# Performance work log

Measured on AMD Instinct MI355X. Metric: run time of the kernel, lower is better.

Reference implementation:

```python
import jax, jax.numpy as jnp
import numpy as np

INTRA_K = 16
OUTER_K = 16
MAX_PAIR = 1024


def _mahalanobis(x, cov_inv, mean):
    # x: (..., D) difference vectors; returns squared Mahalanobis-style form (...,)
    xc = x - mean
    return jnp.einsum('...i,ij,...j->...', xc, cov_inv, xc)


def setup_inputs() -> dict:
    key = jax.random.key(0)
    k1, k2, k3 = jax.random.split(key, 3)
    B, N, M = 4, 1024, 1024
    outputs = jax.random.normal(k1, (B, N, 9), dtype=jnp.float32)
    targets = jax.random.normal(k2, (B, M, 9), dtype=jnp.float32)
    mask = jax.random.randint(k3, (B, M), 0, 2).astype(bool)
    return {"outputs": outputs, "targets": targets, "mask": mask}


def reference(outputs, targets, mask):
    y_pred = outputs[:, :MAX_PAIR]                      # (B, N, 9)
    m = mask.astype(y_pred.dtype)                       # (B, M)
    cnt = m.sum()

    # mean / covariance over masked true grasps (equivalent to boolean-gather)
    mean = (targets * m[..., None]).sum((0, 1)) / cnt   # (9,)
    centered = (targets - mean) * m[..., None]          # masked rows contribute 0
    flat = centered.reshape(-1, 9)
    cov = flat.T @ flat / (cnt - 1.0)                   # (9, 9)
    cov_inv = jnp.linalg.pinv(cov)

    # intra loss: true-vs-pred pairwise distances, masked rows excluded
    diff = targets[:, :, None, :] - y_pred[:, None, :, :]   # (B, M, N, 9)
    d = _mahalanobis(diff, cov_inv, mean)                   # (B, M, N)
    neg_topk, _ = jax.lax.top_k(-d, INTRA_K)                # k smallest
    row_sum = (-neg_topk).sum(-1)                           # (B, M)
    intra_loss = (row_sum * m).sum() / cnt                  # mean over masked rows

    # outer loss: pred-vs-pred pairwise distances, no mask
    diff_r = y_pred[:, None, :, :] - y_pred[:, :, None, :]  # (B, N, N, 9); [b,i,j] = pred[b,j]-pred[b,i]
    d_r = _mahalanobis(diff_r, cov_inv, mean)               # (B, N, N)
    neg_tk, _ = jax.lax.top_k(-d_r, OUTER_K)
    outer_loss = (-neg_tk).mean()

    return intra_loss, intra_loss, outer_loss
```

## Files before the change

### kernel.cpp

```cpp
#include <hip/hip_runtime.h>
#include <math.h>

#define BB   4
#define MM   1024
#define NN   1024
#define DD   9
#define KSEL 16
#define NROW (BB * MM)
#define NSLOT (2 * NROW)
#define NBLK (NSLOT / 4)

struct Ws {
  float yT[BB * DD * NN];
  float qy[BB * NN];
  float rowsum[NSLOT];
  float part[16][55];
  float cnt;
  float mean[DD];
  float cinv[DD * DD];
};

__global__ __launch_bounds__(256) void stats_kernel(
    const float* __restrict__ targets, const int* __restrict__ mask,
    Ws* __restrict__ ws) {
  const int tid = threadIdx.x;
  const int r = blockIdx.x * 256 + tid;

  float acc[55];
#pragma unroll
  for (int k = 0; k < 55; ++k) acc[k] = 0.f;
  if (mask[r] != 0) {
    float t[DD];
#pragma unroll
    for (int k = 0; k < DD; ++k) t[k] = targets[r * DD + k];
    acc[0] = 1.f;
#pragma unroll
    for (int k = 0; k < DD; ++k) acc[1 + k] = t[k];
    int u = 10;
#pragma unroll
    for (int p = 0; p < DD; ++p)
#pragma unroll
      for (int q = p; q < DD; ++q) acc[u++] = t[p] * t[q];
  }

  __shared__ float lds[4][55];
#pragma unroll
  for (int k = 0; k < 55; ++k) {
    float v = acc[k];
#pragma unroll
    for (int off = 32; off > 0; off >>= 1) v += __shfl_down(v, off, 64);
    if ((tid & 63) == 0) lds[tid >> 6][k] = v;
  }
  __syncthreads();
  if (tid < 55)
    ws->part[blockIdx.x][tid] =
        lds[0][tid] + lds[1][tid] + lds[2][tid] + lds[3][tid];
}

__global__ __launch_bounds__(256) void prep_kernel(
    const float* __restrict__ outputs, Ws* __restrict__ ws) {
  const int tid = threadIdx.x;
  __shared__ double Sd[55];
  __shared__ float Cs[DD * DD];

  if (tid < 55) {
    double s = 0.0;
#pragma unroll
    for (int b = 0; b < 16; ++b) s += (double)ws->part[b][tid];
    Sd[tid] = s;
  }
  __syncthreads();

  if (tid < 64) {
    const int lane = tid;
    const double cnt = Sd[0];
    const int p = (lane < DD) ? lane : 0;
    double row[2 * DD];
    {
      const double mu_p = Sd[1 + p] / cnt;
#pragma unroll
      for (int q = 0; q < DD; ++q) {
        const int pp = (p < q) ? p : q;
        const int qq = (p < q) ? q : p;
        const int idx = 10 + 9 * pp - (pp * (pp - 1)) / 2 + (qq - pp);
        row[q] = (Sd[idx] - cnt * mu_p * (Sd[1 + q] / cnt)) / (cnt - 1.0);
        row[DD + q] = (p == q) ? 1.0 : 0.0;
      }
    }
#pragma unroll
    for (int c = 0; c < DD; ++c) {
      const double diag = __shfl(row[c], c, 64);
      const double dinv = 1.0 / diag;
      if (lane == c) {
#pragma unroll
        for (int q = 0; q < 2 * DD; ++q) row[q] *= dinv;
      }
      const double f = (lane == c) ? 0.0 : row[c];
#pragma unroll
      for (int q = 0; q < 2 * DD; ++q) {
        const double pv = __shfl(row[q], c, 64);
        row[q] -= f * pv;
      }
    }
    if (lane < DD) {
#pragma unroll
      for (int q = 0; q < DD; ++q) {
        const float cf = (float)row[DD + q];
        Cs[lane * DD + q] = cf;
        if (blockIdx.x == 0) ws->cinv[lane * DD + q] = cf;
      }
    }
    if (lane == 0 && blockIdx.x == 0) {
      ws->cnt = (float)cnt;
#pragma unroll
      for (int q = 0; q < DD; ++q) ws->mean[q] = (float)(Sd[1 + q] / cnt);
    }
  }
  __syncthreads();

  const int j = blockIdx.x * 256 + tid;
  const int b = j >> 10;
  const int jj = j & (NN - 1);
  float C[DD * DD];
#pragma unroll
  for (int k = 0; k < DD * DD; ++k) C[k] = Cs[k];
  float y[DD];
#pragma unroll
  for (int k = 0; k < DD; ++k) y[k] = outputs[j * DD + k];
  float q = 0.f;
#pragma unroll
  for (int p = 0; p < DD; ++p) {
    float s = 0.f;
#pragma unroll
    for (int t = 0; t < DD; ++t) s += C[p * DD + t] * y[t];
    q += y[p] * s;
    ws->yT[(b * DD + p) * NN + jj] = y[p];
  }
  ws->qy[j] = q;
}

__global__ __launch_bounds__(256) void dist_kernel(
    const float* __restrict__ outputs, const float* __restrict__ targets,
    const int* __restrict__ mask, Ws* __restrict__ ws) {
  const int wv = threadIdx.x >> 6;
  const int lane = threadIdx.x & 63;
  const int s = blockIdx.x * 4 + wv;
  const bool is_intra = (s < NROW);
  const int r = s & (NROW - 1);
  const int b = r >> 10;

  if (is_intra && mask[r] == 0) {
    if (lane == 0) ws->rowsum[s] = 0.f;
    return;
  }

  float a[DD];
  if (is_intra) {
#pragma unroll
    for (int k = 0; k < DD; ++k) a[k] = targets[r * DD + k] - ws->mean[k];
  } else {
#pragma unroll
    for (int k = 0; k < DD; ++k) a[k] = outputs[r * DD + k] + ws->mean[k];
  }
  float w[DD];
  float qa = 0.f;
#pragma unroll
  for (int p = 0; p < DD; ++p) {
    float acc = 0.f;
#pragma unroll
    for (int t = 0; t < DD; ++t) acc += ws->cinv[p * DD + t] * a[t];
    w[p] = acc;
    qa += a[p] * acc;
  }

  float v[16];
#pragma unroll
  for (int k = 0; k < 16; ++k) v[k] = 0.f;
  const float* __restrict__ yTb = ws->yT + (size_t)b * DD * NN;
#pragma unroll
  for (int p = 0; p < DD; ++p) {
    const float4* __restrict__ pl = (const float4*)(yTb + (size_t)p * NN);
#pragma unroll
    for (int c = 0; c < 4; ++c) {
      const float4 y4 = pl[c * 64 + lane];
      v[c * 4 + 0] += w[p] * y4.x;
      v[c * 4 + 1] += w[p] * y4.y;
      v[c * 4 + 2] += w[p] * y4.z;
      v[c * 4 + 3] += w[p] * y4.w;
    }
  }
  {
    const float4* __restrict__ q4 = (const float4*)(ws->qy + (size_t)b * NN);
#pragma unroll
    for (int c = 0; c < 4; ++c) {
      const float4 qv = q4[c * 64 + lane];
      v[c * 4 + 0] = qa + qv.x - 2.f * v[c * 4 + 0];
      v[c * 4 + 1] = qa + qv.y - 2.f * v[c * 4 + 1];
      v[c * 4 + 2] = qa + qv.z - 2.f * v[c * 4 + 2];
      v[c * 4 + 3] = qa + qv.w - 2.f * v[c * 4 + 3];
    }
  }

#pragma unroll
  for (int k = 2; k <= 16; k <<= 1) {
#pragma unroll
    for (int j = k >> 1; j > 0; j >>= 1) {
#pragma unroll
      for (int i = 0; i < 16; ++i) {
        const int l = i ^ j;
        if (l > i) {
          const bool up = ((i & k) == 0);
          const float lo = fminf(v[i], v[l]);
          const float hi = fmaxf(v[i], v[l]);
          v[i] = up ? lo : hi;
          v[l] = up ? hi : lo;
        }
      }
    }
  }

#pragma unroll
  for (int off = 1; off < 64; off <<= 1) {
    float pr[16];
#pragma unroll
    for (int i = 0; i < 16; ++i) pr[i] = __shfl_xor(v[i], off, 64);
#pragma unroll
    for (int i = 0; i < 16; ++i) v[i] = fminf(v[i], pr[15 - i]);
    if (off < 32) {
#pragma unroll
      for (int j = 8; j > 0; j >>= 1) {
#pragma unroll
        for (int i = 0; i < 16; ++i) {
          const int l = i ^ j;
          if (l > i) {
            const float lo = fminf(v[i], v[l]);
            const float hi = fmaxf(v[i], v[l]);
            v[i] = lo;
            v[l] = hi;
          }
        }
      }
    }
  }

  float total = v[0];
#pragma unroll
  for (int k = 1; k < 16; ++k) total += v[k];
  if (lane == 0) ws->rowsum[s] = total;
}

__global__ __launch_bounds__(256) void finalize_kernel(
    const Ws* __restrict__ ws, float* __restrict__ out) {
  const int tid = threadIdx.x;
  double li = 0.0, lo = 0.0;
  for (int k = tid; k < NROW; k += 256) {
    li += (double)ws->rowsum[k];
    lo += (double)ws->rowsum[NROW + k];
  }
#pragma unroll
  for (int off = 32; off > 0; off >>= 1) {
    li += __shfl_down(li, off, 64);
    lo += __shfl_down(lo, off, 64);
  }
  __shared__ double lds_i[4], lds_o[4];
  if ((tid & 63) == 0) {
    lds_i[tid >> 6] = li;
    lds_o[tid >> 6] = lo;
  }
  __syncthreads();
  if (tid == 0) {
    const double si = lds_i[0] + lds_i[1] + lds_i[2] + lds_i[3];
    const double so = lds_o[0] + lds_o[1] + lds_o[2] + lds_o[3];
    const float intra = (float)(si / (double)ws->cnt);
    const float outer = (float)(so / (double)(NROW * KSEL));
    out[0] = intra;
    out[1] = intra;
    out[2] = outer;
  }
}

extern "C" void kernel_launch(void* const* d_in, const int* in_sizes, int n_in,
                              void* d_out, int out_size, void* d_ws,
                              size_t ws_size, hipStream_t stream) {
  const float* outputs = (const float*)d_in[0];
  const float* targets = (const float*)d_in[1];
  const int* mask = (const int*)d_in[2];
  Ws* ws = (Ws*)d_ws;
  float* out = (float*)d_out;

  stats_kernel<<<NROW / 256, 256, 0, stream>>>(targets, mask, ws);
  prep_kernel<<<(BB * NN) / 256, 256, 0, stream>>>(outputs, ws);
  dist_kernel<<<NBLK, 256, 0, stream>>>(outputs, targets, mask, ws);
  finalize_kernel<<<1, 256, 0, stream>>>(ws, out);
}
```

Baseline: 97.23 us.

## Fuse intra/outer rows per wave and fold finalize into dist kernel via ticket

Each wave now handles one target row and one prediction row together, so every load of the transposed predictions and the quadratic terms feeds both distance sets. The separate finalize kernel is replaced by a last-block-done ticket reduction inside the distance kernel, saving a launch. Masked intra rows are no longer skipped early; their top-k is computed and then zeroed, which adds some work. Register pressure roughly doubles, with two 16-value arrays per lane, which may reduce occupancy.

```diff
diff --git a/kernel.cpp b/kernel.cpp
--- a/kernel.cpp
+++ b/kernel.cpp
@@ -1,23 +1,24 @@
 #include <hip/hip_runtime.h>
 #include <math.h>
 
-#define BB   4
-#define MM   1024
-#define NN   1024
-#define DD   9
-#define KSEL 16
-#define NROW (BB * MM)
-#define NSLOT (2 * NROW)
-#define NBLK (NSLOT / 4)
+#define BB    4
+#define MM    1024
+#define NN    1024
+#define DD    9
+#define KSEL  16
+#define NROW  (BB * MM)
+#define NBLKD (NROW / 4)
 
 struct Ws {
   float yT[BB * DD * NN];
   float qy[BB * NN];
-  float rowsum[NSLOT];
+  float bpart_i[NBLKD];
+  float bpart_o[NBLKD];
   float part[16][55];
   float cnt;
   float mean[DD];
   float cinv[DD * DD];
+  unsigned ticket;
 };
 
 __global__ __launch_bounds__(256) void stats_kernel(
@@ -25,6 +26,7 @@
     Ws* __restrict__ ws) {
   const int tid = threadIdx.x;
   const int r = blockIdx.x * 256 + tid;
+  if (blockIdx.x == 0 && tid == 0) ws->ticket = 0u;
 
   float acc[55];
 #pragma unroll
@@ -72,9 +74,8 @@
   __syncthreads();
 
   if (tid < 64) {
-    const int lane = tid;
     const double cnt = Sd[0];
-    const int p = (lane < DD) ? lane : 0;
+    const int p = (tid < DD) ? tid : 0;
     double row[2 * DD];
     {
       const double mu_p = Sd[1 + p] / cnt;
@@ -91,26 +92,26 @@
     for (int c = 0; c < DD; ++c) {
       const double diag = __shfl(row[c], c, 64);
       const double dinv = 1.0 / diag;
-      if (lane == c) {
+      if (tid == c) {
 #pragma unroll
         for (int q = 0; q < 2 * DD; ++q) row[q] *= dinv;
       }
-      const double f = (lane == c) ? 0.0 : row[c];
+      const double f = (tid == c) ? 0.0 : row[c];
 #pragma unroll
       for (int q = 0; q < 2 * DD; ++q) {
         const double pv = __shfl(row[q], c, 64);
         row[q] -= f * pv;
       }
     }
-    if (lane < DD) {
+    if (tid < DD) {
 #pragma unroll
       for (int q = 0; q < DD; ++q) {
         const float cf = (float)row[DD + q];
-        Cs[lane * DD + q] = cf;
-        if (blockIdx.x == 0) ws->cinv[lane * DD + q] = cf;
-      }
-    }
-    if (lane == 0 && blockIdx.x == 0) {
+        Cs[tid * DD + q] = cf;
+        if (blockIdx.x == 0) ws->cinv[tid * DD + q] = cf;
+      }
+    }
+    if (tid == 0 && blockIdx.x == 0) {
       ws->cnt = (float)cnt;
 #pragma unroll
       for (int q = 0; q < DD; ++q) ws->mean[q] = (float)(Sd[1 + q] / cnt);
@@ -121,9 +122,6 @@
   const int j = blockIdx.x * 256 + tid;
   const int b = j >> 10;
   const int jj = j & (NN - 1);
-  float C[DD * DD];
-#pragma unroll
-  for (int k = 0; k < DD * DD; ++k) C[k] = Cs[k];
   float y[DD];
 #pragma unroll
   for (int k = 0; k < DD; ++k) y[k] = outputs[j * DD + k];
@@ -132,75 +130,14 @@
   for (int p = 0; p < DD; ++p) {
     float s = 0.f;
 #pragma unroll
-    for (int t = 0; t < DD; ++t) s += C[p * DD + t] * y[t];
+    for (int t = 0; t < DD; ++t) s += Cs[p * DD + t] * y[t];
     q += y[p] * s;
     ws->yT[(b * DD + p) * NN + jj] = y[p];
   }
   ws->qy[j] = q;
 }
 
-__global__ __launch_bounds__(256) void dist_kernel(
-    const float* __restrict__ outputs, const float* __restrict__ targets,
-    const int* __restrict__ mask, Ws* __restrict__ ws) {
-  const int wv = threadIdx.x >> 6;
-  const int lane = threadIdx.x & 63;
-  const int s = blockIdx.x * 4 + wv;
-  const bool is_intra = (s < NROW);
-  const int r = s & (NROW - 1);
-  const int b = r >> 10;
-
-  if (is_intra && mask[r] == 0) {
-    if (lane == 0) ws->rowsum[s] = 0.f;
-    return;
-  }
-
-  float a[DD];
-  if (is_intra) {
-#pragma unroll
-    for (int k = 0; k < DD; ++k) a[k] = targets[r * DD + k] - ws->mean[k];
-  } else {
-#pragma unroll
-    for (int k = 0; k < DD; ++k) a[k] = outputs[r * DD + k] + ws->mean[k];
-  }
-  float w[DD];
-  float qa = 0.f;
-#pragma unroll
-  for (int p = 0; p < DD; ++p) {
-    float acc = 0.f;
-#pragma unroll
-    for (int t = 0; t < DD; ++t) acc += ws->cinv[p * DD + t] * a[t];
-    w[p] = acc;
-    qa += a[p] * acc;
-  }
-
-  float v[16];
-#pragma unroll
-  for (int k = 0; k < 16; ++k) v[k] = 0.f;
-  const float* __restrict__ yTb = ws->yT + (size_t)b * DD * NN;
-#pragma unroll
-  for (int p = 0; p < DD; ++p) {
-    const float4* __restrict__ pl = (const float4*)(yTb + (size_t)p * NN);
-#pragma unroll
-    for (int c = 0; c < 4; ++c) {
-      const float4 y4 = pl[c * 64 + lane];
-      v[c * 4 + 0] += w[p] * y4.x;
-      v[c * 4 + 1] += w[p] * y4.y;
-      v[c * 4 + 2] += w[p] * y4.z;
-      v[c * 4 + 3] += w[p] * y4.w;
-    }
-  }
-  {
-    const float4* __restrict__ q4 = (const float4*)(ws->qy + (size_t)b * NN);
-#pragma unroll
-    for (int c = 0; c < 4; ++c) {
-      const float4 qv = q4[c * 64 + lane];
-      v[c * 4 + 0] = qa + qv.x - 2.f * v[c * 4 + 0];
-      v[c * 4 + 1] = qa + qv.y - 2.f * v[c * 4 + 1];
-      v[c * 4 + 2] = qa + qv.z - 2.f * v[c * 4 + 2];
-      v[c * 4 + 3] = qa + qv.w - 2.f * v[c * 4 + 3];
-    }
-  }
-
+__device__ __forceinline__ float topk16_sum(float v[16]) {
 #pragma unroll
   for (int k = 2; k <= 16; k <<= 1) {
 #pragma unroll
@@ -218,7 +155,6 @@
       }
     }
   }
-
 #pragma unroll
   for (int off = 1; off < 64; off <<= 1) {
     float pr[16];
@@ -242,40 +178,118 @@
       }
     }
   }
-
-  float total = v[0];
-#pragma unroll
-  for (int k = 1; k < 16; ++k) total += v[k];
-  if (lane == 0) ws->rowsum[s] = total;
-}
-
-__global__ __launch_bounds__(256) void finalize_kernel(
-    const Ws* __restrict__ ws, float* __restrict__ out) {
-  const int tid = threadIdx.x;
-  double li = 0.0, lo = 0.0;
-  for (int k = tid; k < NROW; k += 256) {
-    li += (double)ws->rowsum[k];
-    lo += (double)ws->rowsum[NROW + k];
-  }
-#pragma unroll
-  for (int off = 32; off > 0; off >>= 1) {
-    li += __shfl_down(li, off, 64);
-    lo += __shfl_down(lo, off, 64);
-  }
-  __shared__ double lds_i[4], lds_o[4];
-  if ((tid & 63) == 0) {
-    lds_i[tid >> 6] = li;
-    lds_o[tid >> 6] = lo;
-  }
-  __syncthreads();
-  if (tid == 0) {
-    const double si = lds_i[0] + lds_i[1] + lds_i[2] + lds_i[3];
-    const double so = lds_o[0] + lds_o[1] + lds_o[2] + lds_o[3];
-    const float intra = (float)(si / (double)ws->cnt);
-    const float outer = (float)(so / (double)(NROW * KSEL));
-    out[0] = intra;
-    out[1] = intra;
-    out[2] = outer;
+  float t = v[0];
+#pragma unroll
+  for (int k = 1; k < 16; ++k) t += v[k];
+  return t;
+}
+
+__global__ __launch_bounds__(256) void dist_kernel(
+    const float* __restrict__ outputs, const float* __restrict__ targets,
+    const int* __restrict__ mask, Ws* __restrict__ ws,
+    float* __restrict__ out) {
+  const int wv = threadIdx.x >> 6;
+  const int lane = threadIdx.x & 63;
+  const int r = blockIdx.x * 4 + wv;
+  const int b = r >> 10;
+
+  float ai[DD], ao[DD];
+#pragma unroll
+  for (int k = 0; k < DD; ++k) {
+    const float m = ws->mean[k];
+    ai[k] = targets[r * DD + k] - m;
+    ao[k] = outputs[r * DD + k] + m;
+  }
+  float wi[DD], wo[DD];
+  float qai = 0.f, qao = 0.f;
+#pragma unroll
+  for (int p = 0; p < DD; ++p) {
+    float si = 0.f, so = 0.f;
+#pragma unroll
+    for (int t = 0; t < DD; ++t) {
+      const float c = ws->cinv[p * DD + t];
+      si += c * ai[t];
+      so += c * ao[t];
+    }
+    wi[p] = si;
+    wo[p] = so;
+    qai += ai[p] * si;
+    qao += ao[p] * so;
+  }
+
+  float vi[16], vo[16];
+#pragma unroll
+  for (int k = 0; k < 16; ++k) { vi[k] = 0.f; vo[k] = 0.f; }
+  const float* __restrict__ yTb = ws->yT + (size_t)b * DD * NN;
+#pragma unroll
+  for (int p = 0; p < DD; ++p) {
+    const float4* __restrict__ pl = (const float4*)(yTb + (size_t)p * NN);
+    const float wip = wi[p], wop = wo[p];
+#pragma unroll
+    for (int c = 0; c < 4; ++c) {
+      const float4 y4 = pl[c * 64 + lane];
+      vi[c * 4 + 0] += wip * y4.x; vo[c * 4 + 0] += wop * y4.x;
+      vi[c * 4 + 1] += wip * y4.y; vo[c * 4 + 1] += wop * y4.y;
+      vi[c * 4 + 2] += wip * y4.z; vo[c * 4 + 2] += wop * y4.z;
+      vi[c * 4 + 3] += wip * y4.w; vo[c * 4 + 3] += wop * y4.w;
+    }
+  }
+  {
+    const float4* __restrict__ q4 = (const float4*)(ws->qy + (size_t)b * NN);
+#pragma unroll
+    for (int c = 0; c < 4; ++c) {
+      const float4 qv = q4[c * 64 + lane];
+      vi[c * 4 + 0] = qai + qv.x - 2.f * vi[c * 4 + 0];
+      vi[c * 4 + 1] = qai + qv.y - 2.f * vi[c * 4 + 1];
+      vi[c * 4 + 2] = qai + qv.z - 2.f * vi[c * 4 + 2];
+      vi[c * 4 + 3] = qai + qv.w - 2.f * vi[c * 4 + 3];
+      vo[c * 4 + 0] = qao + qv.x - 2.f * vo[c * 4 + 0];
+      vo[c * 4 + 1] = qao + qv.y - 2.f * vo[c * 4 + 1];
+      vo[c * 4 + 2] = qao + qv.z - 2.f * vo[c * 4 + 2];
+      vo[c * 4 + 3] = qao + qv.w - 2.f * vo[c * 4 + 3];
+    }
+  }
+
+  float tot_i = topk16_sum(vi);
+  float tot_o = topk16_sum(vo);
+  if (mask[r] == 0) tot_i = 0.f;
+
+  __shared__ float s_i[4], s_o[4];
+  __shared__ int s_last;
+  if (lane == 0) { s_i[wv] = tot_i; s_o[wv] = tot_o; }
+  __syncthreads();
+  if (threadIdx.x == 0) {
+    ws->bpart_i[blockIdx.x] = s_i[0] + s_i[1] + s_i[2] + s_i[3];
+    ws->bpart_o[blockIdx.x] = s_o[0] + s_o[1] + s_o[2] + s_o[3];
+    __threadfence();
+    const unsigned t = atomicAdd(&ws->ticket, 1u);
+    s_last = (t == NBLKD - 1) ? 1 : 0;
+  }
+  __syncthreads();
+
+  if (s_last) {
+    double li = 0.0, lo = 0.0;
+    for (int k = threadIdx.x; k < NBLKD; k += 256) {
+      li += (double)atomicAdd(&ws->bpart_i[k], 0.f);
+      lo += (double)atomicAdd(&ws->bpart_o[k], 0.f);
+    }
+#pragma unroll
+    for (int off = 32; off > 0; off >>= 1) {
+      li += __shfl_down(li, off, 64);
+      lo += __shfl_down(lo, off, 64);
+    }
+    __shared__ double ri[4], ro[4];
+    if (lane == 0) { ri[wv] = li; ro[wv] = lo; }
+    __syncthreads();
+    if (threadIdx.x == 0) {
+      const double si = ri[0] + ri[1] + ri[2] + ri[3];
+      const double so = ro[0] + ro[1] + ro[2] + ro[3];
+      const float intra = (float)(si / (double)ws->cnt);
+      const float outer = (float)(so / (double)(NROW * KSEL));
+      out[0] = intra;
+      out[1] = intra;
+      out[2] = outer;
+    }
   }
 }
 
@@ -290,6 +304,5 @@
 
   stats_kernel<<<NROW / 256, 256, 0, stream>>>(targets, mask, ws);
   prep_kernel<<<(BB * NN) / 256, 256, 0, stream>>>(outputs, ws);
-  dist_kernel<<<NBLK, 256, 0, stream>>>(outputs, targets, mask, ws);
-  finalize_kernel<<<1, 256, 0, stream>>>(ws, out);
-}
+  dist_kernel<<<NBLKD, 256, 0, stream>>>(outputs, targets, mask, ws, out);
+}
```

After: 106.9 us. 9.9% more time.
